# Performance work log

Hardware: AMD Instinct MI355X
Metric: run time of the kernel (lower is better)

## Reference

```python
import jax, jax.numpy as jnp
import numpy as np


def setup_inputs() -> dict:
    key = jax.random.key(0)
    ks = jax.random.split(key, 9)
    n, L, H, H2 = 1024, 256, 512, 256
    return {
        "lstms0": jax.random.normal(ks[0], (n, L), jnp.float32),
        "lstms1": jax.random.normal(ks[1], (n, L), jnp.float32),
        "W_foh": jax.random.normal(ks[2], (2 * L, H), jnp.float32) * 0.05,
        "W_fom": jax.random.normal(ks[3], (2 * L, H), jnp.float32) * 0.05,
        "catBias": jax.random.normal(ks[4], (1, 2 * H), jnp.float32) * 0.05,
        "hid2Layer": jax.random.normal(ks[5], (2 * H, H2), jnp.float32) * 0.05,
        "hid2Bias": jax.random.normal(ks[6], (1, H2), jnp.float32) * 0.05,
        "outLayer": jax.random.normal(ks[7], (H2, 1), jnp.float32) * 0.05,
        "outBias": jax.random.normal(ks[8], (1, 1), jnp.float32) * 0.05,
    }


def reference(lstms0, lstms1, W_foh, W_fom, catBias, hid2Layer, hid2Bias, outLayer, outBias):
    act = jnp.tanh
    H = W_foh.shape[1]
    # per-token concatenated BiLSTM state: [n, 2L]
    x = jnp.concatenate([lstms0, lstms1], axis=-1)
    headfov = x @ W_foh  # [n, H]
    modfov = x @ W_fom   # [n, H]
    # activation(concat(head_i, mod_j) + catBias) is elementwise, so it splits:
    ah = act(headfov + catBias[0, :H])  # [n, H]
    am = act(modfov + catBias[0, H:])   # [n, H]
    # concat(ah_i, am_j) @ hid2Layer == ah_i @ W_top + am_j @ W_bot
    A = ah @ hid2Layer[:H]  # [n, H2]
    B = am @ hid2Layer[H:]  # [n, H2]
    # pairwise hidden: [n_head, n_mod, H2]
    Z = act(A[:, None, :] + B[None, :, :] + hid2Bias[0])
    scores = jnp.einsum("ijh,h->ij", Z, outLayer[:, 0]) + outBias[0, 0]
    return scores  # [n, n], scores[i, j] = score(head=i, mod=j)
```

## Files before the change

### kernel.cpp

```cpp
#include <hip/hip_runtime.h>
#include <hip/hip_bf16.h>

typedef short s16x4 __attribute__((ext_vector_type(4)));
typedef short s16x8 __attribute__((ext_vector_type(8)));
typedef float f32x4 __attribute__((ext_vector_type(4)));

#define LOG2E_2 2.8853900817779268f

__device__ __forceinline__ float fexp2(float x){ return __builtin_amdgcn_exp2f(x); }
__device__ __forceinline__ float frcp (float x){ return __builtin_amdgcn_rcpf(x); }
__device__ __forceinline__ float ftanh(float v){
    return 1.0f - 2.0f * frcp(1.0f + fexp2(LOG2E_2 * v));
}
__device__ __forceinline__ unsigned short f2bf(float v){
    __hip_bfloat16 h = __float2bfloat16(v);
    return __builtin_bit_cast(unsigned short, h);
}
__device__ __forceinline__ float bf2f(unsigned short u){
    return __bfloat162float(__builtin_bit_cast(__hip_bfloat16, u));
}
__device__ __forceinline__ f32x4 mfma32(s16x8 a, s16x8 b, f32x4 c){
    return __builtin_amdgcn_mfma_f32_16x16x32_bf16(a, b, c, 0, 0, 0);
}

__global__ __launch_bounds__(256) void prep_x(
    const float* __restrict__ l0, const float* __restrict__ l1,
    unsigned short* __restrict__ xhi, unsigned short* __restrict__ xlo)
{
    int idx = (blockIdx.x * 256 + threadIdx.x) * 4;
    int r = idx >> 9, c = idx & 511;
    float4 v = (c < 256) ? *(const float4*)(l0 + r*256 + c)
                         : *(const float4*)(l1 + r*256 + (c - 256));
    ushort4 h, l;
    h.x = f2bf(v.x); l.x = f2bf(v.x - bf2f(h.x));
    h.y = f2bf(v.y); l.y = f2bf(v.y - bf2f(h.y));
    h.z = f2bf(v.z); l.z = f2bf(v.z - bf2f(h.z));
    h.w = f2bf(v.w); l.w = f2bf(v.w - bf2f(h.w));
    *(ushort4*)(xhi + idx) = h;
    *(ushort4*)(xlo + idx) = l;
}

__global__ __launch_bounds__(256) void prep_wt(
    const float* __restrict__ srcA, const float* __restrict__ srcB,
    int splitN, int lda, int K,
    unsigned short* __restrict__ dhi, unsigned short* __restrict__ dlo)
{
    __shared__ float F[32][33];
    const int t = threadIdx.x;
    const int k0 = blockIdx.x * 32, n0 = blockIdx.y * 32;
    {
        int kk = t >> 3, n4 = (t & 7) * 4;
        int n = n0 + n4;
        const float* s = (n < splitN) ? (srcA + (k0+kk)*lda + n)
                                      : (srcB + (k0+kk)*lda + (n - splitN));
        float4 v = *(const float4*)s;
        F[kk][n4+0] = v.x; F[kk][n4+1] = v.y; F[kk][n4+2] = v.z; F[kk][n4+3] = v.w;
    }
    __syncthreads();
    {
        int nn = t >> 3, k4 = (t & 7) * 4;
        ushort4 h, l;
        float v0 = F[k4+0][nn]; h.x = f2bf(v0); l.x = f2bf(v0 - bf2f(h.x));
        float v1 = F[k4+1][nn]; h.y = f2bf(v1); l.y = f2bf(v1 - bf2f(h.y));
        float v2 = F[k4+2][nn]; h.z = f2bf(v2); l.z = f2bf(v2 - bf2f(h.z));
        float v3 = F[k4+3][nn]; h.w = f2bf(v3); l.w = f2bf(v3 - bf2f(h.w));
        *(ushort4*)(dhi + (n0+nn)*K + k0 + k4) = h;
        *(ushort4*)(dlo + (n0+nn)*K + k0 + k4) = l;
    }
}

__global__ __launch_bounds__(256) void k1_mfma(
    const unsigned short* __restrict__ xhi, const unsigned short* __restrict__ xlo,
    const unsigned short* __restrict__ whi, const unsigned short* __restrict__ wlo,
    const float* __restrict__ cb,
    unsigned short* __restrict__ hvhi, unsigned short* __restrict__ hvlo)
{
    __shared__ unsigned short Ah[64][40], Al[64][40], Bh[32][40], Bl[32][40];
    const int t = threadIdx.x;
    const int r0 = blockIdx.y * 64, c0 = blockIdx.x * 32;
    const int w = t >> 6, lane = t & 63;
    const int m = lane & 15, quad = lane >> 4;

    const int arow = t >> 2, aseg = t & 3;
    const int brow = (t & 127) >> 2, bseg = t & 3;
    const bool doB = (t < 128);

    f32x4 acc0 = {0,0,0,0}, acc1 = {0,0,0,0};

    const unsigned short* pAh = xhi + (r0+arow)*512 + aseg*8;
    const unsigned short* pAl = xlo + (r0+arow)*512 + aseg*8;
    const unsigned short* pBh = whi + (c0+brow)*512 + bseg*8;
    const unsigned short* pBl = wlo + (c0+brow)*512 + bseg*8;

    uint4 pah = *(const uint4*)pAh;
    uint4 pal = *(const uint4*)pAl;
    uint4 pbh = {}, pbl = {};
    if (doB) { pbh = *(const uint4*)pBh; pbl = *(const uint4*)pBl; }

    for (int c = 0; c < 16; ++c) {
        __syncthreads();
        *(uint4*)&Ah[arow][aseg*8] = pah;
        *(uint4*)&Al[arow][aseg*8] = pal;
        if (doB) {
            *(uint4*)&Bh[brow][bseg*8] = pbh;
            *(uint4*)&Bl[brow][bseg*8] = pbl;
        }
        __syncthreads();
        if (c + 1 < 16) {
            int k0 = (c+1) * 32;
            pah = *(const uint4*)(pAh + k0);
            pal = *(const uint4*)(pAl + k0);
            if (doB) {
                pbh = *(const uint4*)(pBh + k0);
                pbl = *(const uint4*)(pBl + k0);
            }
        }
        {
            const int ko = quad*8;
            s16x8 ah  = *(const s16x8*)&Ah[w*16 + m][ko];
            s16x8 al  = *(const s16x8*)&Al[w*16 + m][ko];
            s16x8 b0h = *(const s16x8*)&Bh[m][ko];
            s16x8 b0l = *(const s16x8*)&Bl[m][ko];
            s16x8 b1h = *(const s16x8*)&Bh[16 + m][ko];
            s16x8 b1l = *(const s16x8*)&Bl[16 + m][ko];
            acc0 = mfma32(ah, b0h, acc0);
            acc0 = mfma32(ah, b0l, acc0);
            acc0 = mfma32(al, b0h, acc0);
            acc1 = mfma32(ah, b1h, acc1);
            acc1 = mfma32(ah, b1l, acc1);
            acc1 = mfma32(al, b1h, acc1);
        }
    }

    #pragma unroll
    for (int nt = 0; nt < 2; ++nt) {
        f32x4 a = nt ? acc1 : acc0;
        const int col = c0 + nt*16 + m;
        const float bias = cb[col];
        #pragma unroll
        for (int reg = 0; reg < 4; ++reg) {
            const int row = r0 + w*16 + quad*4 + reg;
            float v = ftanh(a[reg] + bias);
            unsigned short h = f2bf(v);
            unsigned short l = f2bf(v - bf2f(h));
            hvhi[row*1024 + col] = h;
            hvlo[row*1024 + col] = l;
        }
    }
}

__global__ __launch_bounds__(256) void k2_mfma(
    const unsigned short* __restrict__ hvhi, const unsigned short* __restrict__ hvlo,
    const unsigned short* __restrict__ w2hi, const unsigned short* __restrict__ w2lo,
    const float* __restrict__ h2b, float* __restrict__ P)
{
    __shared__ unsigned short Ah[64][40], Al[64][40], Bh[32][40], Bl[32][40];
    const int t = threadIdx.x;
    const int r0 = blockIdx.y * 64, c0 = blockIdx.x * 32;
    const int half = (c0 >= 256) ? 1 : 0;
    const int ho = half * 512;
    const int nw = c0 & 255;
    const int w = t >> 6, lane = t & 63;
    const int m = lane & 15, quad = lane >> 4;

    const int arow = t >> 2, aseg = t & 3;
    const int brow = (t & 127) >> 2, bseg = t & 3;
    const bool doB = (t < 128);

    f32x4 acc0 = {0,0,0,0}, acc1 = {0,0,0,0};

    const unsigned short* pAh = hvhi + (r0+arow)*1024 + ho + aseg*8;
    const unsigned short* pAl = hvlo + (r0+arow)*1024 + ho + aseg*8;
    const unsigned short* pBh = w2hi + (nw+brow)*1024 + ho + bseg*8;
    const unsigned short* pBl = w2lo + (nw+brow)*1024 + ho + bseg*8;

    uint4 pah = *(const uint4*)pAh;
    uint4 pal = *(const uint4*)pAl;
    uint4 pbh = {}, pbl = {};
    if (doB) { pbh = *(const uint4*)pBh; pbl = *(const uint4*)pBl; }

    for (int c = 0; c < 16; ++c) {
        __syncthreads();
        *(uint4*)&Ah[arow][aseg*8] = pah;
        *(uint4*)&Al[arow][aseg*8] = pal;
        if (doB) {
            *(uint4*)&Bh[brow][bseg*8] = pbh;
            *(uint4*)&Bl[brow][bseg*8] = pbl;
        }
        __syncthreads();
        if (c + 1 < 16) {
            int k0 = (c+1) * 32;
            pah = *(const uint4*)(pAh + k0);
            pal = *(const uint4*)(pAl + k0);
            if (doB) {
                pbh = *(const uint4*)(pBh + k0);
                pbl = *(const uint4*)(pBl + k0);
            }
        }
        {
            const int ko = quad*8;
            s16x8 ah  = *(const s16x8*)&Ah[w*16 + m][ko];
            s16x8 al  = *(const s16x8*)&Al[w*16 + m][ko];
            s16x8 b0h = *(const s16x8*)&Bh[m][ko];
            s16x8 b0l = *(const s16x8*)&Bl[m][ko];
            s16x8 b1h = *(const s16x8*)&Bh[16 + m][ko];
            s16x8 b1l = *(const s16x8*)&Bl[16 + m][ko];
            acc0 = mfma32(ah, b0h, acc0);
            acc0 = mfma32(ah, b0l, acc0);
            acc0 = mfma32(al, b0h, acc0);
            acc1 = mfma32(ah, b1h, acc1);
            acc1 = mfma32(ah, b1l, acc1);
            acc1 = mfma32(al, b1h, acc1);
        }
    }

    #pragma unroll
    for (int nt = 0; nt < 2; ++nt) {
        f32x4 a = nt ? acc1 : acc0;
        const int col = c0 + nt*16 + m;
        const float bias = half ? 0.0f : h2b[col];
        #pragma unroll
        for (int reg = 0; reg < 4; ++reg) {
            const int row = r0 + w*16 + quad*4 + reg;
            P[row*512 + col] = fexp2((a[reg] + bias) * LOG2E_2);
        }
    }
}

__global__ __launch_bounds__(256) void k3_pairwise(
    const float* __restrict__ P, const float* __restrict__ w,
    const float* __restrict__ ob, float* __restrict__ out)
{
    __shared__ float As[32][68];
    __shared__ float Bs[64][34];
    __shared__ float wls[256];
    const int tid = threadIdx.x;
    const int tx = tid & 15;
    const int ty = tid >> 4;
    const int i0 = blockIdx.y * 32, j0 = blockIdx.x * 32;

    wls[tid] = w[tid];

    int rr0 = tid >> 4,        c40 = (tid & 15) * 4;
    int rr1 = (tid + 256) >> 4, c41 = (tid & 15) * 4;

    float acc[2][2] = {};

    float4 pa0 = *(const float4*)&P[(i0+rr0)*512 + 0 + c40];
    float4 pa1 = *(const float4*)&P[(i0+rr1)*512 + 0 + c41];
    float4 pb0 = *(const float4*)&P[(j0+rr0)*512 + 256 + 0 + c40];
    float4 pb1 = *(const float4*)&P[(j0+rr1)*512 + 256 + 0 + c41];

    for (int c = 0; c < 4; ++c) {
        __syncthreads();
        *(float4*)&As[rr0][c40] = pa0;
        *(float4*)&As[rr1][c41] = pa1;
        Bs[c40+0][rr0] = pb0.x; Bs[c40+1][rr0] = pb0.y;
        Bs[c40+2][rr0] = pb0.z; Bs[c40+3][rr0] = pb0.w;
        Bs[c41+0][rr1] = pb1.x; Bs[c41+1][rr1] = pb1.y;
        Bs[c41+2][rr1] = pb1.z; Bs[c41+3][rr1] = pb1.w;
        __syncthreads();
        if (c + 1 < 4) {
            int h0 = (c+1) * 64;
            pa0 = *(const float4*)&P[(i0+rr0)*512 + h0 + c40];
            pa1 = *(const float4*)&P[(i0+rr1)*512 + h0 + c41];
            pb0 = *(const float4*)&P[(j0+rr0)*512 + 256 + h0 + c40];
            pb1 = *(const float4*)&P[(j0+rr1)*512 + 256 + h0 + c41];
        }

        for (int hh = 0; hh < 64; hh += 4) {
            float4 wv = *(const float4*)&wls[c*64 + hh];
            float4 a0 = *(const float4*)&As[ty*2+0][hh];
            float4 a1 = *(const float4*)&As[ty*2+1][hh];
            float2 b0 = *(const float2*)&Bs[hh+0][tx*2];
            float2 b1 = *(const float2*)&Bs[hh+1][tx*2];
            float2 b2 = *(const float2*)&Bs[hh+2][tx*2];
            float2 b3 = *(const float2*)&Bs[hh+3][tx*2];
            float aa[2][4] = {{a0.x,a0.y,a0.z,a0.w},{a1.x,a1.y,a1.z,a1.w}};
            float bb[4][2] = {{b0.x,b0.y},{b1.x,b1.y},{b2.x,b2.y},{b3.x,b3.y}};
            float ww[4] = {wv.x, wv.y, wv.z, wv.w};
            #pragma unroll
            for (int h = 0; h < 4; ++h)
                #pragma unroll
                for (int r = 0; r < 2; ++r)
                    #pragma unroll
                    for (int q = 0; q < 2; ++q) {
                        float u = fmaf(aa[r][h], bb[h][q], 1.0f);
                        acc[r][q] = fmaf(ww[h], frcp(u), acc[r][q]);
                    }
        }
    }

    float sumw = 0.0f;
    #pragma unroll
    for (int h = 0; h < 256; h += 4) {
        float4 wv = *(const float4*)&wls[h];
        sumw += (wv.x + wv.y) + (wv.z + wv.w);
    }
    const float base = ob[0] + sumw;
    const int row = i0 + ty*2;
    const int col = j0 + tx*2;
    #pragma unroll
    for (int r = 0; r < 2; ++r) {
        float2 o;
        o.x = base - 2.0f*acc[r][0];
        o.y = base - 2.0f*acc[r][1];
        *(float2*)&out[(row+r)*1024 + col] = o;
    }
}

extern "C" void kernel_launch(void* const* d_in, const int* in_sizes, int n_in,
                              void* d_out, int out_size, void* d_ws, size_t ws_size,
                              hipStream_t stream) {
    const float* l0   = (const float*)d_in[0];
    const float* l1   = (const float*)d_in[1];
    const float* Wfoh = (const float*)d_in[2];
    const float* Wfom = (const float*)d_in[3];
    const float* cb   = (const float*)d_in[4];
    const float* W2   = (const float*)d_in[5];
    const float* h2b  = (const float*)d_in[6];
    const float* w    = (const float*)d_in[7];
    const float* ob   = (const float*)d_in[8];
    float* out = (float*)d_out;

    unsigned short* hv_hi  = (unsigned short*)d_ws;
    unsigned short* hv_lo  = hv_hi + 1024*1024;
    float*          P      = (float*)(hv_lo + 1024*1024);
    unsigned short* xs_hi  = (unsigned short*)(P + 1024*512);
    unsigned short* xs_lo  = xs_hi + 1024*512;
    unsigned short* w1t_hi = xs_lo + 1024*512;
    unsigned short* w1t_lo = w1t_hi + 1024*512;
    unsigned short* w2t_hi = w1t_lo + 1024*512;
    unsigned short* w2t_lo = w2t_hi + 256*1024;

    prep_x<<<512, 256, 0, stream>>>(l0, l1, xs_hi, xs_lo);
    prep_wt<<<dim3(16,32), 256, 0, stream>>>(Wfoh, Wfom, 512, 512, 512, w1t_hi, w1t_lo);
    prep_wt<<<dim3(32,8),  256, 0, stream>>>(W2, W2, 1<<30, 256, 1024, w2t_hi, w2t_lo);
    k1_mfma<<<dim3(32,16), 256, 0, stream>>>(xs_hi, xs_lo, w1t_hi, w1t_lo, cb, hv_hi, hv_lo);
    k2_mfma<<<dim3(16,16), 256, 0, stream>>>(hv_hi, hv_lo, w2t_hi, w2t_lo, h2b, P);
    k3_pairwise<<<dim3(32,32), 256, 0, stream>>>(P, w, ob, out);
}
```

Baseline: 131.6 us.

## Batch four reciprocals into one, enlarge pairwise tile, merge prep kernels

The pairwise kernel now adds four weighted reciprocal terms as a single fraction. This replaces four rcp ops with one plus extra multiplies, cutting transcendental throughput pressure. The tile grows to 64x32 with 4x2 outputs per thread and B is stored row-major, so reads are float4. The three prep kernels become one launch. The risk is overflow or precision loss from multiplying four denominators, plus higher register use.

Result: no change. 129.1 us (-1.9%).

```diff
diff --git a/kernel.cpp b/kernel.cpp
--- a/kernel.cpp
+++ b/kernel.cpp
@@ -1,7 +1,6 @@
 #include <hip/hip_runtime.h>
 #include <hip/hip_bf16.h>
 
-typedef short s16x4 __attribute__((ext_vector_type(4)));
 typedef short s16x8 __attribute__((ext_vector_type(8)));
 typedef float f32x4 __attribute__((ext_vector_type(4)));
 
@@ -23,31 +22,47 @@
     return __builtin_amdgcn_mfma_f32_16x16x32_bf16(a, b, c, 0, 0, 0);
 }
 
-__global__ __launch_bounds__(256) void prep_x(
+__global__ __launch_bounds__(256) void prep_all(
     const float* __restrict__ l0, const float* __restrict__ l1,
-    unsigned short* __restrict__ xhi, unsigned short* __restrict__ xlo)
-{
-    int idx = (blockIdx.x * 256 + threadIdx.x) * 4;
-    int r = idx >> 9, c = idx & 511;
-    float4 v = (c < 256) ? *(const float4*)(l0 + r*256 + c)
-                         : *(const float4*)(l1 + r*256 + (c - 256));
-    ushort4 h, l;
-    h.x = f2bf(v.x); l.x = f2bf(v.x - bf2f(h.x));
-    h.y = f2bf(v.y); l.y = f2bf(v.y - bf2f(h.y));
-    h.z = f2bf(v.z); l.z = f2bf(v.z - bf2f(h.z));
-    h.w = f2bf(v.w); l.w = f2bf(v.w - bf2f(h.w));
-    *(ushort4*)(xhi + idx) = h;
-    *(ushort4*)(xlo + idx) = l;
-}
-
-__global__ __launch_bounds__(256) void prep_wt(
-    const float* __restrict__ srcA, const float* __restrict__ srcB,
-    int splitN, int lda, int K,
-    unsigned short* __restrict__ dhi, unsigned short* __restrict__ dlo)
+    const float* __restrict__ Wfoh, const float* __restrict__ Wfom,
+    const float* __restrict__ W2,
+    unsigned short* __restrict__ xhi, unsigned short* __restrict__ xlo,
+    unsigned short* __restrict__ w1hi, unsigned short* __restrict__ w1lo,
+    unsigned short* __restrict__ w2hi, unsigned short* __restrict__ w2lo)
 {
     __shared__ float F[32][33];
     const int t = threadIdx.x;
-    const int k0 = blockIdx.x * 32, n0 = blockIdx.y * 32;
+    const int bid = blockIdx.x;
+
+    if (bid < 512) {
+        int idx = (bid * 256 + t) * 4;
+        int r = idx >> 9, c = idx & 511;
+        float4 v = (c < 256) ? *(const float4*)(l0 + r*256 + c)
+                             : *(const float4*)(l1 + r*256 + (c - 256));
+        ushort4 h, l;
+        h.x = f2bf(v.x); l.x = f2bf(v.x - bf2f(h.x));
+        h.y = f2bf(v.y); l.y = f2bf(v.y - bf2f(h.y));
+        h.z = f2bf(v.z); l.z = f2bf(v.z - bf2f(h.z));
+        h.w = f2bf(v.w); l.w = f2bf(v.w - bf2f(h.w));
+        *(ushort4*)(xhi + idx) = h;
+        *(ushort4*)(xlo + idx) = l;
+        return;
+    }
+
+    const float* srcA; const float* srcB;
+    int splitN, lda, K, k0, n0;
+    unsigned short *dhi, *dlo;
+    if (bid < 1024) {
+        int b = bid - 512;
+        k0 = (b & 15) * 32; n0 = (b >> 4) * 32;
+        srcA = Wfoh; srcB = Wfom; splitN = 512; lda = 512; K = 512;
+        dhi = w1hi; dlo = w1lo;
+    } else {
+        int b = bid - 1024;
+        k0 = (b & 31) * 32; n0 = (b >> 5) * 32;
+        srcA = W2; srcB = W2; splitN = 1 << 30; lda = 256; K = 1024;
+        dhi = w2hi; dlo = w2lo;
+    }
     {
         int kk = t >> 3, n4 = (t & 7) * 4;
         int n = n0 + n4;
@@ -231,63 +246,68 @@
     const float* __restrict__ P, const float* __restrict__ w,
     const float* __restrict__ ob, float* __restrict__ out)
 {
-    __shared__ float As[32][68];
-    __shared__ float Bs[64][34];
+    __shared__ float As[64][68];
+    __shared__ float Bs[32][68];
     __shared__ float wls[256];
     const int tid = threadIdx.x;
     const int tx = tid & 15;
     const int ty = tid >> 4;
-    const int i0 = blockIdx.y * 32, j0 = blockIdx.x * 32;
+    const int i0 = blockIdx.y * 64, j0 = blockIdx.x * 32;
 
     wls[tid] = w[tid];
 
-    int rr0 = tid >> 4,        c40 = (tid & 15) * 4;
-    int rr1 = (tid + 256) >> 4, c41 = (tid & 15) * 4;
-
-    float acc[2][2] = {};
-
-    float4 pa0 = *(const float4*)&P[(i0+rr0)*512 + 0 + c40];
-    float4 pa1 = *(const float4*)&P[(i0+rr1)*512 + 0 + c41];
-    float4 pb0 = *(const float4*)&P[(j0+rr0)*512 + 256 + 0 + c40];
-    float4 pb1 = *(const float4*)&P[(j0+rr1)*512 + 256 + 0 + c41];
+    const int ar = tid >> 2, ac = (tid & 3) * 16;
+    const int br = tid >> 3, bc = (tid & 7) * 8;
+
+    const float* pA = P + (i0 + ar) * 512 + ac;
+    const float* pB = P + (j0 + br) * 512 + 256 + bc;
+
+    float acc[4][2] = {};
+    float4 ra[4], rb[2];
+    #pragma unroll
+    for (int k = 0; k < 4; ++k) ra[k] = *(const float4*)(pA + k*4);
+    #pragma unroll
+    for (int k = 0; k < 2; ++k) rb[k] = *(const float4*)(pB + k*4);
 
     for (int c = 0; c < 4; ++c) {
         __syncthreads();
-        *(float4*)&As[rr0][c40] = pa0;
-        *(float4*)&As[rr1][c41] = pa1;
-        Bs[c40+0][rr0] = pb0.x; Bs[c40+1][rr0] = pb0.y;
-        Bs[c40+2][rr0] = pb0.z; Bs[c40+3][rr0] = pb0.w;
-        Bs[c41+0][rr1] = pb1.x; Bs[c41+1][rr1] = pb1.y;
-        Bs[c41+2][rr1] = pb1.z; Bs[c41+3][rr1] = pb1.w;
+        #pragma unroll
+        for (int k = 0; k < 4; ++k) *(float4*)&As[ar][ac + k*4] = ra[k];
+        #pragma unroll
+        for (int k = 0; k < 2; ++k) *(float4*)&Bs[br][bc + k*4] = rb[k];
         __syncthreads();
         if (c + 1 < 4) {
-            int h0 = (c+1) * 64;
-            pa0 = *(const float4*)&P[(i0+rr0)*512 + h0 + c40];
-            pa1 = *(const float4*)&P[(i0+rr1)*512 + h0 + c41];
-            pb0 = *(const float4*)&P[(j0+rr0)*512 + 256 + h0 + c40];
-            pb1 = *(const float4*)&P[(j0+rr1)*512 + 256 + h0 + c41];
-        }
-
+            int off = (c + 1) * 64;
+            #pragma unroll
+            for (int k = 0; k < 4; ++k) ra[k] = *(const float4*)(pA + off + k*4);
+            #pragma unroll
+            for (int k = 0; k < 2; ++k) rb[k] = *(const float4*)(pB + off + k*4);
+        }
+
+        #pragma unroll 2
         for (int hh = 0; hh < 64; hh += 4) {
             float4 wv = *(const float4*)&wls[c*64 + hh];
-            float4 a0 = *(const float4*)&As[ty*2+0][hh];
-            float4 a1 = *(const float4*)&As[ty*2+1][hh];
-            float2 b0 = *(const float2*)&Bs[hh+0][tx*2];
-            float2 b1 = *(const float2*)&Bs[hh+1][tx*2];
-            float2 b2 = *(const float2*)&Bs[hh+2][tx*2];
-            float2 b3 = *(const float2*)&Bs[hh+3][tx*2];
-            float aa[2][4] = {{a0.x,a0.y,a0.z,a0.w},{a1.x,a1.y,a1.z,a1.w}};
-            float bb[4][2] = {{b0.x,b0.y},{b1.x,b1.y},{b2.x,b2.y},{b3.x,b3.y}};
-            float ww[4] = {wv.x, wv.y, wv.z, wv.w};
-            #pragma unroll
-            for (int h = 0; h < 4; ++h)
+            float4 av[4];
+            #pragma unroll
+            for (int r = 0; r < 4; ++r) av[r] = *(const float4*)&As[ty*4 + r][hh];
+            float4 bv[2];
+            #pragma unroll
+            for (int q = 0; q < 2; ++q) bv[q] = *(const float4*)&Bs[tx + 16*q][hh];
+            #pragma unroll
+            for (int r = 0; r < 4; ++r)
                 #pragma unroll
-                for (int r = 0; r < 2; ++r)
-                    #pragma unroll
-                    for (int q = 0; q < 2; ++q) {
-                        float u = fmaf(aa[r][h], bb[h][q], 1.0f);
-                        acc[r][q] = fmaf(ww[h], frcp(u), acc[r][q]);
-                    }
+                for (int q = 0; q < 2; ++q) {
+                    float u0 = fmaf(av[r].x, bv[q].x, 1.0f);
+                    float u1 = fmaf(av[r].y, bv[q].y, 1.0f);
+                    float u2 = fmaf(av[r].z, bv[q].z, 1.0f);
+                    float u3 = fmaf(av[r].w, bv[q].w, 1.0f);
+                    float d01 = u0 * u1;
+                    float d23 = u2 * u3;
+                    float p01 = fmaf(wv.x, u1, wv.y * u0);
+                    float p23 = fmaf(wv.z, u3, wv.w * u2);
+                    float num = fmaf(p01, d23, p23 * d01);
+                    acc[r][q] = fmaf(num, frcp(d01 * d23), acc[r][q]);
+                }
         }
     }
 
@@ -298,14 +318,11 @@
         sumw += (wv.x + wv.y) + (wv.z + wv.w);
     }
     const float base = ob[0] + sumw;
-    const int row = i0 + ty*2;
-    const int col = j0 + tx*2;
-    #pragma unroll
-    for (int r = 0; r < 2; ++r) {
-        float2 o;
-        o.x = base - 2.0f*acc[r][0];
-        o.y = base - 2.0f*acc[r][1];
-        *(float2*)&out[(row+r)*1024 + col] = o;
+    #pragma unroll
+    for (int r = 0; r < 4; ++r) {
+        const int row = i0 + ty*4 + r;
+        out[row*1024 + j0 + tx]      = base - 2.0f * acc[r][0];
+        out[row*1024 + j0 + tx + 16] = base - 2.0f * acc[r][1];
     }
 }
 
@@ -333,10 +350,9 @@
     unsigned short* w2t_hi = w1t_lo + 1024*512;
     unsigned short* w2t_lo = w2t_hi + 256*1024;
 
-    prep_x<<<512, 256, 0, stream>>>(l0, l1, xs_hi, xs_lo);
-    prep_wt<<<dim3(16,32), 256, 0, stream>>>(Wfoh, Wfom, 512, 512, 512, w1t_hi, w1t_lo);
-    prep_wt<<<dim3(32,8),  256, 0, stream>>>(W2, W2, 1<<30, 256, 1024, w2t_hi, w2t_lo);
+    prep_all<<<1280, 256, 0, stream>>>(l0, l1, Wfoh, Wfom, W2,
+                                       xs_hi, xs_lo, w1t_hi, w1t_lo, w2t_hi, w2t_lo);
     k1_mfma<<<dim3(32,16), 256, 0, stream>>>(xs_hi, xs_lo, w1t_hi, w1t_lo, cb, hv_hi, hv_lo);
     k2_mfma<<<dim3(16,16), 256, 0, stream>>>(hv_hi, hv_lo, w2t_hi, w2t_lo, h2b, P);
-    k3_pairwise<<<dim3(32,32), 256, 0, stream>>>(P, w, ob, out);
-}
+    k3_pairwise<<<dim3(32,16), 256, 0, stream>>>(P, w, ob, out);
+}
```
